# Optimization experiments

Hardware: AMD Instinct MI355X
Metric: run time of the kernel (lower is better)

## Reference

```python
import jax, jax.numpy as jnp
import numpy as np

BETA = 0.25

def setup_inputs() -> dict:
    key = jax.random.key(0)
    k1, k2, k3, k4 = jax.random.split(key, 4)
    B, C, H, W = 8, 4, 64, 64
    K = 8192
    return {
        'z_e_in': jax.random.normal(k1, (B, C, H, W), dtype=jnp.float32),
        'pq_w': jax.random.normal(k2, (C, C), dtype=jnp.float32) * 0.5,
        'pq_b': jax.random.normal(k3, (C,), dtype=jnp.float32) * 0.1,
        'codebook': jax.random.normal(k4, (K, C), dtype=jnp.float32),
    }

def reference(z_e_in, pq_w, pq_b, codebook):
    # pre_quant_conv: 1x1 conv == channel-mixing matmul
    z_e = jnp.einsum('bchw,oc->bohw', z_e_in, pq_w) + pq_b[None, :, None, None]
    B, C, H, W = z_e.shape
    z = z_e.transpose(0, 2, 3, 1).reshape(B, H * W, C)  # [B, HW, C]
    # squared Euclidean distances (argmin is invariant to sqrt in torch.cdist)
    d2 = (jnp.sum(z * z, axis=-1, keepdims=True)
          - 2.0 * jnp.einsum('bnc,kc->bnk', z, codebook)
          + jnp.sum(codebook * codebook, axis=-1))  # [B, HW, K]
    idx = jnp.argmin(d2, axis=-1)                    # [B, HW]
    z_q = codebook[idx]                               # gather, [B, HW, C]
    z_flat = z.reshape(-1, C)
    zq_flat = z_q.reshape(-1, C)
    sg = jax.lax.stop_gradient
    commitment_loss = jnp.mean((sg(zq_flat) - z_flat) ** 2)
    codebook_loss = jnp.mean((zq_flat - sg(z_flat)) ** 2)
    q_loss = codebook_loss + BETA * commitment_loss
    # straight-through estimator
    zq_st = z_flat + sg(zq_flat - z_flat)
    latent = zq_st.reshape(B, H, W, C).transpose(0, 3, 1, 2)  # [B, C, H, W]
    return latent, q_loss
```

## Files before the change

### kernel.cpp

```cpp
#include <hip/hip_runtime.h>
#include <math.h>

#define N_POINTS 32768
#define KCODES   8192
#define HW       4096
#define CHW      16384
#define NSEG     64
#define SEGLEN   (KCODES / NSEG)
#define PPT      8
#define PTILE    (256 * PPT)

#define WS_CB2    0
#define WS_CBN    131072
#define WS_PACKED 163840

__device__ __forceinline__ void compute_z(
    const float* __restrict__ ze, const float* __restrict__ w,
    const float* __restrict__ bias, int n, float zo[4], float& zz) {
  int b = n >> 12, hw = n & 4095;
  const float* p = ze + b * CHW + hw;
  float x0 = p[0], x1 = p[HW], x2 = p[2 * HW], x3 = p[3 * HW];
#pragma unroll
  for (int o = 0; o < 4; ++o) {
    float acc = __fmul_rn(x0, w[o * 4 + 0]);
    acc = __fadd_rn(acc, __fmul_rn(x1, w[o * 4 + 1]));
    acc = __fadd_rn(acc, __fmul_rn(x2, w[o * 4 + 2]));
    acc = __fadd_rn(acc, __fmul_rn(x3, w[o * 4 + 3]));
    zo[o] = __fadd_rn(acc, bias[o]);
  }
  float s = __fmul_rn(zo[0], zo[0]);
  s = __fadd_rn(s, __fmul_rn(zo[1], zo[1]));
  s = __fadd_rn(s, __fmul_rn(zo[2], zo[2]));
  s = __fadd_rn(s, __fmul_rn(zo[3], zo[3]));
  zz = s;
}

__global__ __launch_bounds__(256) void vq_init(
    const float* __restrict__ cb, float4* __restrict__ cb2,
    float* __restrict__ cbn, unsigned long long* __restrict__ packed,
    float* __restrict__ out) {
  int t = blockIdx.x * 256 + threadIdx.x;
  packed[t] = 0xFFFFFFFFFFFFFFFFull;
  if (t < KCODES) {
    float c0 = cb[t * 4 + 0], c1 = cb[t * 4 + 1];
    float c2 = cb[t * 4 + 2], c3 = cb[t * 4 + 3];
    cb2[t] = make_float4(2.f * c0, 2.f * c1, 2.f * c2, 2.f * c3);
    float s = __fmul_rn(c0, c0);
    s = __fadd_rn(s, __fmul_rn(c1, c1));
    s = __fadd_rn(s, __fmul_rn(c2, c2));
    s = __fadd_rn(s, __fmul_rn(c3, c3));
    cbn[t] = s;
  }
  if (t == 0) out[N_POINTS * 4] = 0.f;
}

__global__ __launch_bounds__(256, 3) void vq_scan(
    const float* __restrict__ ze, const float* __restrict__ w,
    const float* __restrict__ bias, const float4* __restrict__ cb2,
    const float* __restrict__ cbn, unsigned long long* __restrict__ packed) {
  __shared__ float4 s_c[SEGLEN];
  __shared__ float  s_n[SEGLEN];
  int tid = threadIdx.x;
  int k0 = blockIdx.y * SEGLEN;
  ((float*)s_c)[tid]       = ((const float*)(cb2 + k0))[tid];
  ((float*)s_c)[tid + 256] = ((const float*)(cb2 + k0))[tid + 256];
  if (tid < SEGLEN) s_n[tid] = cbn[k0 + tid];
  int n0 = blockIdx.x * PTILE + tid;
  float z[PPT][4], zz[PPT], best[PPT];
  int bidx[PPT];
#pragma unroll
  for (int p = 0; p < PPT; ++p) {
    compute_z(ze, w, bias, n0 + 256 * p, z[p], zz[p]);
    best[p] = INFINITY;
    bidx[p] = 0;
  }
  __syncthreads();
  float4 cA[4], nA;
  cA[0] = s_c[0]; cA[1] = s_c[1]; cA[2] = s_c[2]; cA[3] = s_c[3];
  nA = *(const float4*)&s_n[0];
  for (int kc = 0; kc < SEGLEN; kc += 4) {
    int kn = (kc + 4) & (SEGLEN - 1);
    float4 cB[4], nB;
    cB[0] = s_c[kn + 0]; cB[1] = s_c[kn + 1];
    cB[2] = s_c[kn + 2]; cB[3] = s_c[kn + 3];
    nB = *(const float4*)&s_n[kn];
    float cnr[4] = {nA.x, nA.y, nA.z, nA.w};
#pragma unroll
    for (int r = 0; r < 4; ++r) {
      int kk = k0 + kc + r;
#pragma unroll
      for (int p = 0; p < PPT; ++p) {
        float d = __fmul_rn(z[p][0], cA[r].x);
        d = __fadd_rn(d, __fmul_rn(z[p][1], cA[r].y));
        d = __fadd_rn(d, __fmul_rn(z[p][2], cA[r].z));
        d = __fadd_rn(d, __fmul_rn(z[p][3], cA[r].w));
        float s = __fadd_rn(__fsub_rn(zz[p], d), cnr[r]);
        if (s < best[p]) { best[p] = s; bidx[p] = kk; }
      }
    }
    cA[0] = cB[0]; cA[1] = cB[1]; cA[2] = cB[2]; cA[3] = cB[3];
    nA = nB;
  }
#pragma unroll
  for (int p = 0; p < PPT; ++p) {
    unsigned int u = __float_as_uint(best[p]);
    unsigned int so = (u & 0x80000000u) ? ~u : (u | 0x80000000u);
    unsigned long long key =
        ((unsigned long long)so << 32) | (unsigned int)bidx[p];
    atomicMin(&packed[n0 + 256 * p], key);
  }
}

__global__ __launch_bounds__(256) void vq_finish(
    const float* __restrict__ ze, const float* __restrict__ w,
    const float* __restrict__ bias, const float* __restrict__ cb,
    const unsigned long long* __restrict__ packed, float* __restrict__ out) {
  int n = blockIdx.x * 256 + threadIdx.x;
  int bidx = (unsigned int)(packed[n] & 0xFFFFFFFFull);
  float4 c = ((const float4*)cb)[bidx];
  int b = n >> 12, hw = n & 4095;
  float* o = out + b * CHW + hw;
  o[0] = c.x; o[HW] = c.y; o[2 * HW] = c.z; o[3 * HW] = c.w;
  float z[4], zz;
  compute_z(ze, w, bias, n, z, zz);
  float d0 = c.x - z[0], d1 = c.y - z[1], d2 = c.z - z[2], d3 = c.w - z[3];
  float e = d0 * d0 + d1 * d1 + d2 * d2 + d3 * d3;
#pragma unroll
  for (int off = 32; off > 0; off >>= 1) e += __shfl_down(e, off, 64);
  __shared__ float sred[4];
  if ((threadIdx.x & 63) == 0) sred[threadIdx.x >> 6] = e;
  __syncthreads();
  if (threadIdx.x == 0) {
    float t = (sred[0] + sred[1]) + (sred[2] + sred[3]);
    atomicAdd(out + (N_POINTS * 4), t * (1.25f / 131072.f));
  }
}

extern "C" void kernel_launch(void* const* d_in, const int* in_sizes, int n_in,
                              void* d_out, int out_size, void* d_ws, size_t ws_size,
                              hipStream_t stream) {
  const float* ze   = (const float*)d_in[0];
  const float* w    = (const float*)d_in[1];
  const float* bias = (const float*)d_in[2];
  const float* cb   = (const float*)d_in[3];

  char* ws = (char*)d_ws;
  float4* cb2 = (float4*)(ws + WS_CB2);
  float*  cbn = (float*)(ws + WS_CBN);
  unsigned long long* packed = (unsigned long long*)(ws + WS_PACKED);
  float* out = (float*)d_out;

  vq_init<<<128, 256, 0, stream>>>(cb, cb2, cbn, packed, out);
  vq_scan<<<dim3(N_POINTS / PTILE, NSEG), 256, 0, stream>>>(
      ze, w, bias, cb2, cbn, packed);
  vq_finish<<<128, 256, 0, stream>>>(ze, w, bias, cb, packed, out);
}
```

Measured before the change: 116.0 us.

## Fuse scan and finish into one kernel with per-wave codebook slices

Replaces the segmented scan with packed 64-bit atomicMin and the separate finish kernel with a single kernel. Each 512-thread block handles 64 points, each wave scans a uniform 1024-code slice read directly from global memory, and waves reduce in shared memory before the gather and loss. This removes the packed workspace initialization, the atomics, and one launch. In exchange, each thread processes one point instead of eight, which reduces register reuse of codebook loads and instruction-level parallelism.

```diff
diff --git a/kernel.cpp b/kernel.cpp
--- a/kernel.cpp
+++ b/kernel.cpp
@@ -5,14 +5,12 @@
 #define KCODES   8192
 #define HW       4096
 #define CHW      16384
-#define NSEG     64
-#define SEGLEN   (KCODES / NSEG)
-#define PPT      8
-#define PTILE    (256 * PPT)
+#define NWAVES   8
+#define SLICE    (KCODES / NWAVES)
+#define CHUNK    8
 
-#define WS_CB2    0
-#define WS_CBN    131072
-#define WS_PACKED 163840
+#define WS_CB2 0
+#define WS_CBN 131072
 
 __device__ __forceinline__ void compute_z(
     const float* __restrict__ ze, const float* __restrict__ w,
@@ -35,104 +33,85 @@
   zz = s;
 }
 
-__global__ __launch_bounds__(256) void vq_init(
+__global__ __launch_bounds__(256) void vq_prep(
     const float* __restrict__ cb, float4* __restrict__ cb2,
-    float* __restrict__ cbn, unsigned long long* __restrict__ packed,
-    float* __restrict__ out) {
+    float* __restrict__ cbn, float* __restrict__ out) {
   int t = blockIdx.x * 256 + threadIdx.x;
-  packed[t] = 0xFFFFFFFFFFFFFFFFull;
-  if (t < KCODES) {
-    float c0 = cb[t * 4 + 0], c1 = cb[t * 4 + 1];
-    float c2 = cb[t * 4 + 2], c3 = cb[t * 4 + 3];
-    cb2[t] = make_float4(2.f * c0, 2.f * c1, 2.f * c2, 2.f * c3);
-    float s = __fmul_rn(c0, c0);
-    s = __fadd_rn(s, __fmul_rn(c1, c1));
-    s = __fadd_rn(s, __fmul_rn(c2, c2));
-    s = __fadd_rn(s, __fmul_rn(c3, c3));
-    cbn[t] = s;
-  }
+  float c0 = cb[t * 4 + 0], c1 = cb[t * 4 + 1];
+  float c2 = cb[t * 4 + 2], c3 = cb[t * 4 + 3];
+  cb2[t] = make_float4(2.f * c0, 2.f * c1, 2.f * c2, 2.f * c3);
+  float s = __fmul_rn(c0, c0);
+  s = __fadd_rn(s, __fmul_rn(c1, c1));
+  s = __fadd_rn(s, __fmul_rn(c2, c2));
+  s = __fadd_rn(s, __fmul_rn(c3, c3));
+  cbn[t] = s;
   if (t == 0) out[N_POINTS * 4] = 0.f;
 }
 
-__global__ __launch_bounds__(256, 3) void vq_scan(
-    const float* __restrict__ ze, const float* __restrict__ w,
-    const float* __restrict__ bias, const float4* __restrict__ cb2,
-    const float* __restrict__ cbn, unsigned long long* __restrict__ packed) {
-  __shared__ float4 s_c[SEGLEN];
-  __shared__ float  s_n[SEGLEN];
-  int tid = threadIdx.x;
-  int k0 = blockIdx.y * SEGLEN;
-  ((float*)s_c)[tid]       = ((const float*)(cb2 + k0))[tid];
-  ((float*)s_c)[tid + 256] = ((const float*)(cb2 + k0))[tid + 256];
-  if (tid < SEGLEN) s_n[tid] = cbn[k0 + tid];
-  int n0 = blockIdx.x * PTILE + tid;
-  float z[PPT][4], zz[PPT], best[PPT];
-  int bidx[PPT];
-#pragma unroll
-  for (int p = 0; p < PPT; ++p) {
-    compute_z(ze, w, bias, n0 + 256 * p, z[p], zz[p]);
-    best[p] = INFINITY;
-    bidx[p] = 0;
-  }
-  __syncthreads();
-  float4 cA[4], nA;
-  cA[0] = s_c[0]; cA[1] = s_c[1]; cA[2] = s_c[2]; cA[3] = s_c[3];
-  nA = *(const float4*)&s_n[0];
-  for (int kc = 0; kc < SEGLEN; kc += 4) {
-    int kn = (kc + 4) & (SEGLEN - 1);
-    float4 cB[4], nB;
-    cB[0] = s_c[kn + 0]; cB[1] = s_c[kn + 1];
-    cB[2] = s_c[kn + 2]; cB[3] = s_c[kn + 3];
-    nB = *(const float4*)&s_n[kn];
-    float cnr[4] = {nA.x, nA.y, nA.z, nA.w};
-#pragma unroll
-    for (int r = 0; r < 4; ++r) {
-      int kk = k0 + kc + r;
-#pragma unroll
-      for (int p = 0; p < PPT; ++p) {
-        float d = __fmul_rn(z[p][0], cA[r].x);
-        d = __fadd_rn(d, __fmul_rn(z[p][1], cA[r].y));
-        d = __fadd_rn(d, __fmul_rn(z[p][2], cA[r].z));
-        d = __fadd_rn(d, __fmul_rn(z[p][3], cA[r].w));
-        float s = __fadd_rn(__fsub_rn(zz[p], d), cnr[r]);
-        if (s < best[p]) { best[p] = s; bidx[p] = kk; }
-      }
-    }
-    cA[0] = cB[0]; cA[1] = cB[1]; cA[2] = cB[2]; cA[3] = cB[3];
-    nA = nB;
-  }
-#pragma unroll
-  for (int p = 0; p < PPT; ++p) {
-    unsigned int u = __float_as_uint(best[p]);
-    unsigned int so = (u & 0x80000000u) ? ~u : (u | 0x80000000u);
-    unsigned long long key =
-        ((unsigned long long)so << 32) | (unsigned int)bidx[p];
-    atomicMin(&packed[n0 + 256 * p], key);
-  }
-}
-
-__global__ __launch_bounds__(256) void vq_finish(
+__global__ __launch_bounds__(512, 4) void vq_main(
     const float* __restrict__ ze, const float* __restrict__ w,
     const float* __restrict__ bias, const float* __restrict__ cb,
-    const unsigned long long* __restrict__ packed, float* __restrict__ out) {
-  int n = blockIdx.x * 256 + threadIdx.x;
-  int bidx = (unsigned int)(packed[n] & 0xFFFFFFFFull);
-  float4 c = ((const float4*)cb)[bidx];
-  int b = n >> 12, hw = n & 4095;
-  float* o = out + b * CHW + hw;
-  o[0] = c.x; o[HW] = c.y; o[2 * HW] = c.z; o[3 * HW] = c.w;
+    const float4* __restrict__ cb2, const float* __restrict__ cbn,
+    float* __restrict__ out) {
+  int tid  = threadIdx.x;
+  int lane = tid & 63;
+  int wv   = __builtin_amdgcn_readfirstlane(tid >> 6);
+  int n    = blockIdx.x * 64 + lane;
+
   float z[4], zz;
   compute_z(ze, w, bias, n, z, zz);
-  float d0 = c.x - z[0], d1 = c.y - z[1], d2 = c.z - z[2], d3 = c.w - z[3];
-  float e = d0 * d0 + d1 * d1 + d2 * d2 + d3 * d3;
+
+  const float4* cseg = cb2 + (wv << 10);
+  const float*  nseg = cbn + (wv << 10);
+  int kbase = wv << 10;
+  float best = INFINITY;
+  int bidx = 0;
+
+  for (int kc = 0; kc < SLICE; kc += CHUNK) {
+    float4 cc[CHUNK];
+    float  cn[CHUNK];
 #pragma unroll
-  for (int off = 32; off > 0; off >>= 1) e += __shfl_down(e, off, 64);
-  __shared__ float sred[4];
-  if ((threadIdx.x & 63) == 0) sred[threadIdx.x >> 6] = e;
+    for (int j = 0; j < CHUNK; ++j) cc[j] = cseg[kc + j];
+#pragma unroll
+    for (int j = 0; j < CHUNK; ++j) cn[j] = nseg[kc + j];
+#pragma unroll
+    for (int j = 0; j < CHUNK; ++j) {
+      float d = __fmul_rn(z[0], cc[j].x);
+      d = __fadd_rn(d, __fmul_rn(z[1], cc[j].y));
+      d = __fadd_rn(d, __fmul_rn(z[2], cc[j].z));
+      d = __fadd_rn(d, __fmul_rn(z[3], cc[j].w));
+      float s = __fadd_rn(__fsub_rn(zz, d), cn[j]);
+      if (s < best) { best = s; bidx = kbase + kc + j; }
+    }
+  }
+
+  unsigned int u  = __float_as_uint(best);
+  unsigned int so = (u & 0x80000000u) ? ~u : (u | 0x80000000u);
+  unsigned long long key =
+      ((unsigned long long)so << 32) | (unsigned int)bidx;
+
+  __shared__ unsigned long long red[NWAVES][64];
+  red[wv][lane] = key;
   __syncthreads();
-  if (threadIdx.x == 0) {
-    float t = (sred[0] + sred[1]) + (sred[2] + sred[3]);
-    atomicAdd(out + (N_POINTS * 4), t * (1.25f / 131072.f));
+
+  if (tid < 64) {
+    unsigned long long m = red[0][lane];
+#pragma unroll
+    for (int i = 1; i < NWAVES; ++i) {
+      unsigned long long v = red[i][lane];
+      if (v < m) m = v;
+    }
+    int idx = (int)(unsigned int)(m & 0xFFFFFFFFull);
+    float4 c = ((const float4*)cb)[idx];
+    int b = n >> 12, hw = n & 4095;
+    float* o = out + b * CHW + hw;
+    o[0] = c.x; o[HW] = c.y; o[2 * HW] = c.z; o[3 * HW] = c.w;
+    float d0 = c.x - z[0], d1 = c.y - z[1];
+    float d2 = c.z - z[2], d3 = c.w - z[3];
+    float e = d0 * d0 + d1 * d1 + d2 * d2 + d3 * d3;
+#pragma unroll
+    for (int off = 32; off > 0; off >>= 1) e += __shfl_down(e, off, 64);
+    if (lane == 0) atomicAdd(out + (N_POINTS * 4), e * (1.25f / 131072.f));
   }
 }
 
@@ -147,11 +126,8 @@
   char* ws = (char*)d_ws;
   float4* cb2 = (float4*)(ws + WS_CB2);
   float*  cbn = (float*)(ws + WS_CBN);
-  unsigned long long* packed = (unsigned long long*)(ws + WS_PACKED);
   float* out = (float*)d_out;
 
-  vq_init<<<128, 256, 0, stream>>>(cb, cb2, cbn, packed, out);
-  vq_scan<<<dim3(N_POINTS / PTILE, NSEG), 256, 0, stream>>>(
-      ze, w, bias, cb2, cbn, packed);
-  vq_finish<<<128, 256, 0, stream>>>(ze, w, bias, cb, packed, out);
+  vq_prep<<<32, 256, 0, stream>>>(cb, cb2, cbn, out);
+  vq_main<<<N_POINTS / 64, 512, 0, stream>>>(ze, w, bias, cb, cb2, cbn, out);
 }
```

New measurement: 147.2 us. 26.9% more time.

## Fold codebook prep into scan, use packed FP32 math and SoA shared layout

Applied to the files above, without the earlier changes.

Removes the separate init kernel: each scan block computes the scaled codebook (-2c) and code norms for its segment directly into shared memory, stored as structure-of-arrays. The inner distance loop uses v_pk_mul/v_pk_add packed FP32 instructions to evaluate two codes per instruction, with z broadcast into pairs. Block size goes to 512 with 4 points per thread, and the packed-key and loss initialisation move to hipMemsetAsync. The aim is to halve the VALU instruction count in the hot loop and drop one launch, at the cost of inline asm that may hinder scheduling, plus extra memset calls.

```diff
diff --git a/kernel.cpp b/kernel.cpp
--- a/kernel.cpp
+++ b/kernel.cpp
@@ -5,14 +5,29 @@
 #define KCODES   8192
 #define HW       4096
 #define CHW      16384
-#define NSEG     64
-#define SEGLEN   (KCODES / NSEG)
-#define PPT      8
-#define PTILE    (256 * PPT)
 
-#define WS_CB2    0
-#define WS_CBN    131072
-#define WS_PACKED 163840
+#define NSEG    64
+#define SEGLEN  (KCODES / NSEG)
+#define PPT     4
+#define BLOCK   512
+#define PTILE   (BLOCK * PPT)
+#define GRIDX   (N_POINTS / PTILE)
+
+#define WS_PACKED 0
+
+typedef float f2 __attribute__((ext_vector_type(2)));
+typedef float f4 __attribute__((ext_vector_type(4)));
+
+static __device__ __forceinline__ f2 pk_mul(f2 a, f2 b) {
+  f2 d;
+  asm("v_pk_mul_f32 %0, %1, %2" : "=v"(d) : "v"(a), "v"(b));
+  return d;
+}
+static __device__ __forceinline__ f2 pk_add(f2 a, f2 b) {
+  f2 d;
+  asm("v_pk_add_f32 %0, %1, %2" : "=v"(d) : "v"(a), "v"(b));
+  return d;
+}
 
 __device__ __forceinline__ void compute_z(
     const float* __restrict__ ze, const float* __restrict__ w,
@@ -35,79 +50,76 @@
   zz = s;
 }
 
-__global__ __launch_bounds__(256) void vq_init(
-    const float* __restrict__ cb, float4* __restrict__ cb2,
-    float* __restrict__ cbn, unsigned long long* __restrict__ packed,
-    float* __restrict__ out) {
-  int t = blockIdx.x * 256 + threadIdx.x;
-  packed[t] = 0xFFFFFFFFFFFFFFFFull;
-  if (t < KCODES) {
-    float c0 = cb[t * 4 + 0], c1 = cb[t * 4 + 1];
-    float c2 = cb[t * 4 + 2], c3 = cb[t * 4 + 3];
-    cb2[t] = make_float4(2.f * c0, 2.f * c1, 2.f * c2, 2.f * c3);
-    float s = __fmul_rn(c0, c0);
-    s = __fadd_rn(s, __fmul_rn(c1, c1));
-    s = __fadd_rn(s, __fmul_rn(c2, c2));
-    s = __fadd_rn(s, __fmul_rn(c3, c3));
-    cbn[t] = s;
-  }
-  if (t == 0) out[N_POINTS * 4] = 0.f;
-}
-
-__global__ __launch_bounds__(256, 3) void vq_scan(
+__global__ __launch_bounds__(512, 4) void vq_scan(
     const float* __restrict__ ze, const float* __restrict__ w,
-    const float* __restrict__ bias, const float4* __restrict__ cb2,
-    const float* __restrict__ cbn, unsigned long long* __restrict__ packed) {
-  __shared__ float4 s_c[SEGLEN];
-  __shared__ float  s_n[SEGLEN];
+    const float* __restrict__ bias, const float* __restrict__ cb,
+    unsigned long long* __restrict__ packed) {
+  __shared__ float sm[5][SEGLEN] __attribute__((aligned(16)));
   int tid = threadIdx.x;
   int k0 = blockIdx.y * SEGLEN;
-  ((float*)s_c)[tid]       = ((const float*)(cb2 + k0))[tid];
-  ((float*)s_c)[tid + 256] = ((const float*)(cb2 + k0))[tid + 256];
-  if (tid < SEGLEN) s_n[tid] = cbn[k0 + tid];
+
+  if (tid < SEGLEN) {
+    f4 c = ((const f4*)cb)[k0 + tid];
+    sm[0][tid] = __fmul_rn(-2.f, c.x);
+    sm[1][tid] = __fmul_rn(-2.f, c.y);
+    sm[2][tid] = __fmul_rn(-2.f, c.z);
+    sm[3][tid] = __fmul_rn(-2.f, c.w);
+    float cn = __fmul_rn(c.x, c.x);
+    cn = __fadd_rn(cn, __fmul_rn(c.y, c.y));
+    cn = __fadd_rn(cn, __fmul_rn(c.z, c.z));
+    cn = __fadd_rn(cn, __fmul_rn(c.w, c.w));
+    sm[4][tid] = cn;
+  }
+
   int n0 = blockIdx.x * PTILE + tid;
-  float z[PPT][4], zz[PPT], best[PPT];
+  f2 zd[PPT][4], zzd[PPT];
+  float best[PPT];
   int bidx[PPT];
 #pragma unroll
   for (int p = 0; p < PPT; ++p) {
-    compute_z(ze, w, bias, n0 + 256 * p, z[p], zz[p]);
+    float z[4], zz;
+    compute_z(ze, w, bias, n0 + BLOCK * p, z, zz);
+#pragma unroll
+    for (int c = 0; c < 4; ++c) zd[p][c] = (f2){z[c], z[c]};
+    zzd[p] = (f2){zz, zz};
     best[p] = INFINITY;
     bidx[p] = 0;
   }
   __syncthreads();
-  float4 cA[4], nA;
-  cA[0] = s_c[0]; cA[1] = s_c[1]; cA[2] = s_c[2]; cA[3] = s_c[3];
-  nA = *(const float4*)&s_n[0];
-  for (int kc = 0; kc < SEGLEN; kc += 4) {
-    int kn = (kc + 4) & (SEGLEN - 1);
-    float4 cB[4], nB;
-    cB[0] = s_c[kn + 0]; cB[1] = s_c[kn + 1];
-    cB[2] = s_c[kn + 2]; cB[3] = s_c[kn + 3];
-    nB = *(const float4*)&s_n[kn];
-    float cnr[4] = {nA.x, nA.y, nA.z, nA.w};
+
+#pragma unroll 2
+  for (int j = 0; j < SEGLEN; j += 4) {
+    f4 q0 = *(const f4*)&sm[0][j];
+    f4 q1 = *(const f4*)&sm[1][j];
+    f4 q2 = *(const f4*)&sm[2][j];
+    f4 q3 = *(const f4*)&sm[3][j];
+    f4 qn = *(const f4*)&sm[4][j];
 #pragma unroll
-    for (int r = 0; r < 4; ++r) {
-      int kk = k0 + kc + r;
-#pragma unroll
-      for (int p = 0; p < PPT; ++p) {
-        float d = __fmul_rn(z[p][0], cA[r].x);
-        d = __fadd_rn(d, __fmul_rn(z[p][1], cA[r].y));
-        d = __fadd_rn(d, __fmul_rn(z[p][2], cA[r].z));
-        d = __fadd_rn(d, __fmul_rn(z[p][3], cA[r].w));
-        float s = __fadd_rn(__fsub_rn(zz[p], d), cnr[r]);
-        if (s < best[p]) { best[p] = s; bidx[p] = kk; }
-      }
+    for (int p = 0; p < PPT; ++p) {
+      f2 dA = pk_mul(zd[p][0], q0.xy);
+      dA = pk_add(dA, pk_mul(zd[p][1], q1.xy));
+      dA = pk_add(dA, pk_mul(zd[p][2], q2.xy));
+      dA = pk_add(dA, pk_mul(zd[p][3], q3.xy));
+      f2 sA = pk_add(pk_add(zzd[p], dA), qn.xy);
+      f2 dB = pk_mul(zd[p][0], q0.zw);
+      dB = pk_add(dB, pk_mul(zd[p][1], q1.zw));
+      dB = pk_add(dB, pk_mul(zd[p][2], q2.zw));
+      dB = pk_add(dB, pk_mul(zd[p][3], q3.zw));
+      f2 sB = pk_add(pk_add(zzd[p], dB), qn.zw);
+      if (sA.x < best[p]) { best[p] = sA.x; bidx[p] = j + 0; }
+      if (sA.y < best[p]) { best[p] = sA.y; bidx[p] = j + 1; }
+      if (sB.x < best[p]) { best[p] = sB.x; bidx[p] = j + 2; }
+      if (sB.y < best[p]) { best[p] = sB.y; bidx[p] = j + 3; }
     }
-    cA[0] = cB[0]; cA[1] = cB[1]; cA[2] = cB[2]; cA[3] = cB[3];
-    nA = nB;
   }
+
 #pragma unroll
   for (int p = 0; p < PPT; ++p) {
     unsigned int u = __float_as_uint(best[p]);
     unsigned int so = (u & 0x80000000u) ? ~u : (u | 0x80000000u);
     unsigned long long key =
-        ((unsigned long long)so << 32) | (unsigned int)bidx[p];
-    atomicMin(&packed[n0 + 256 * p], key);
+        ((unsigned long long)so << 32) | (unsigned int)(k0 + bidx[p]);
+    atomicMin(&packed[n0 + BLOCK * p], key);
   }
 }
 
@@ -144,14 +156,13 @@
   const float* bias = (const float*)d_in[2];
   const float* cb   = (const float*)d_in[3];
 
-  char* ws = (char*)d_ws;
-  float4* cb2 = (float4*)(ws + WS_CB2);
-  float*  cbn = (float*)(ws + WS_CBN);
-  unsigned long long* packed = (unsigned long long*)(ws + WS_PACKED);
+  unsigned long long* packed =
+      (unsigned long long*)((char*)d_ws + WS_PACKED);
   float* out = (float*)d_out;
 
-  vq_init<<<128, 256, 0, stream>>>(cb, cb2, cbn, packed, out);
-  vq_scan<<<dim3(N_POINTS / PTILE, NSEG), 256, 0, stream>>>(
-      ze, w, bias, cb2, cbn, packed);
+  hipMemsetAsync(packed, 0xFF, N_POINTS * sizeof(unsigned long long), stream);
+  hipMemsetAsync((char*)d_out + (size_t)N_POINTS * 4 * sizeof(float), 0,
+                 sizeof(float), stream);
+  vq_scan<<<dim3(GRIDX, NSEG), BLOCK, 0, stream>>>(ze, w, bias, cb, packed);
   vq_finish<<<128, 256, 0, stream>>>(ze, w, bias, cb, packed, out);
 }
```

Result: slower. 128.8 us (+11.0%).

## Fold codebook prep into scan, use single-wave blocks and memsets

Applied to the files above, without the earlier changes.

Removes the separate init kernel. Each scan block now computes the doubled codebook entries and their norms directly from the raw codebook into shared memory, and the packed buffer and loss slot are cleared with hipMemsetAsync. Scan blocks shrink to one 64-thread wave each, so the block-wide __syncthreads becomes a wave barrier and the grid gains four times as many blocks along x. This is meant to cut a kernel launch and sync cost and improve load balance, at the price of redundant codebook preprocessing per block and memset overheads.

```diff
diff --git a/kernel.cpp b/kernel.cpp
--- a/kernel.cpp
+++ b/kernel.cpp
@@ -8,11 +8,10 @@
 #define NSEG     64
 #define SEGLEN   (KCODES / NSEG)
 #define PPT      8
-#define PTILE    (256 * PPT)
+#define PTILE    (64 * PPT)
+#define GRIDX    (N_POINTS / PTILE)
 
-#define WS_CB2    0
-#define WS_CBN    131072
-#define WS_PACKED 163840
+#define WS_PACKED 0
 
 __device__ __forceinline__ void compute_z(
     const float* __restrict__ ze, const float* __restrict__ w,
@@ -35,46 +34,35 @@
   zz = s;
 }
 
-__global__ __launch_bounds__(256) void vq_init(
-    const float* __restrict__ cb, float4* __restrict__ cb2,
-    float* __restrict__ cbn, unsigned long long* __restrict__ packed,
-    float* __restrict__ out) {
-  int t = blockIdx.x * 256 + threadIdx.x;
-  packed[t] = 0xFFFFFFFFFFFFFFFFull;
-  if (t < KCODES) {
-    float c0 = cb[t * 4 + 0], c1 = cb[t * 4 + 1];
-    float c2 = cb[t * 4 + 2], c3 = cb[t * 4 + 3];
-    cb2[t] = make_float4(2.f * c0, 2.f * c1, 2.f * c2, 2.f * c3);
-    float s = __fmul_rn(c0, c0);
-    s = __fadd_rn(s, __fmul_rn(c1, c1));
-    s = __fadd_rn(s, __fmul_rn(c2, c2));
-    s = __fadd_rn(s, __fmul_rn(c3, c3));
-    cbn[t] = s;
-  }
-  if (t == 0) out[N_POINTS * 4] = 0.f;
-}
-
-__global__ __launch_bounds__(256, 3) void vq_scan(
+__global__ __launch_bounds__(64, 4) void vq_scan(
     const float* __restrict__ ze, const float* __restrict__ w,
-    const float* __restrict__ bias, const float4* __restrict__ cb2,
-    const float* __restrict__ cbn, unsigned long long* __restrict__ packed) {
+    const float* __restrict__ bias, const float* __restrict__ cb,
+    unsigned long long* __restrict__ packed) {
   __shared__ float4 s_c[SEGLEN];
   __shared__ float  s_n[SEGLEN];
-  int tid = threadIdx.x;
+  int lane = threadIdx.x;
   int k0 = blockIdx.y * SEGLEN;
-  ((float*)s_c)[tid]       = ((const float*)(cb2 + k0))[tid];
-  ((float*)s_c)[tid + 256] = ((const float*)(cb2 + k0))[tid + 256];
-  if (tid < SEGLEN) s_n[tid] = cbn[k0 + tid];
-  int n0 = blockIdx.x * PTILE + tid;
+#pragma unroll
+  for (int q = 0; q < 2; ++q) {
+    float4 c = ((const float4*)cb)[k0 + 64 * q + lane];
+    s_c[64 * q + lane] =
+        make_float4(2.f * c.x, 2.f * c.y, 2.f * c.z, 2.f * c.w);
+    float s = __fmul_rn(c.x, c.x);
+    s = __fadd_rn(s, __fmul_rn(c.y, c.y));
+    s = __fadd_rn(s, __fmul_rn(c.z, c.z));
+    s = __fadd_rn(s, __fmul_rn(c.w, c.w));
+    s_n[64 * q + lane] = s;
+  }
+  int n0 = blockIdx.x * PTILE + lane;
   float z[PPT][4], zz[PPT], best[PPT];
   int bidx[PPT];
 #pragma unroll
   for (int p = 0; p < PPT; ++p) {
-    compute_z(ze, w, bias, n0 + 256 * p, z[p], zz[p]);
+    compute_z(ze, w, bias, n0 + 64 * p, z[p], zz[p]);
     best[p] = INFINITY;
     bidx[p] = 0;
   }
-  __syncthreads();
+  __builtin_amdgcn_wave_barrier();
   float4 cA[4], nA;
   cA[0] = s_c[0]; cA[1] = s_c[1]; cA[2] = s_c[2]; cA[3] = s_c[3];
   nA = *(const float4*)&s_n[0];
@@ -107,7 +95,7 @@
     unsigned int so = (u & 0x80000000u) ? ~u : (u | 0x80000000u);
     unsigned long long key =
         ((unsigned long long)so << 32) | (unsigned int)bidx[p];
-    atomicMin(&packed[n0 + 256 * p], key);
+    atomicMin(&packed[n0 + 64 * p], key);
   }
 }
 
@@ -144,14 +132,13 @@
   const float* bias = (const float*)d_in[2];
   const float* cb   = (const float*)d_in[3];
 
-  char* ws = (char*)d_ws;
-  float4* cb2 = (float4*)(ws + WS_CB2);
-  float*  cbn = (float*)(ws + WS_CBN);
-  unsigned long long* packed = (unsigned long long*)(ws + WS_PACKED);
+  unsigned long long* packed =
+      (unsigned long long*)((char*)d_ws + WS_PACKED);
   float* out = (float*)d_out;
 
-  vq_init<<<128, 256, 0, stream>>>(cb, cb2, cbn, packed, out);
-  vq_scan<<<dim3(N_POINTS / PTILE, NSEG), 256, 0, stream>>>(
-      ze, w, bias, cb2, cbn, packed);
+  hipMemsetAsync(packed, 0xFF, N_POINTS * sizeof(unsigned long long), stream);
+  hipMemsetAsync((char*)d_out + (size_t)N_POINTS * 4 * sizeof(float), 0,
+                 sizeof(float), stream);
+  vq_scan<<<dim3(GRIDX, NSEG), 64, 0, stream>>>(ze, w, bias, cb, packed);
   vq_finish<<<128, 256, 0, stream>>>(ze, w, bias, cb, packed, out);
 }
```

After: 117.2 us. No clear change (+1.1%).
